# Optimization experiments

Measured on AMD Instinct MI355X. Metric: run time of the kernel, lower is better.

## Reference

```python
import jax, jax.numpy as jnp
import numpy as np
import math

DIM_K = 64  # head dim used for scaling
NEG = -1000000000.0

def setup_inputs() -> dict:
    key = jax.random.key(0)
    k1, k2, k3, k4 = jax.random.split(key, 4)
    B, H, S, D = 4, 16, 2048, 64
    return {
        "key": jax.random.normal(k1, (B, H, S, D), dtype=jnp.float32),
        "query": jax.random.normal(k2, (B, H, S, D), dtype=jnp.float32),
        "value": jax.random.normal(k3, (B, H, S, D), dtype=jnp.float32),
        "mask": jax.random.randint(k4, (B, S, S), 0, 2, dtype=jnp.int32),
    }

def reference(key, query, value, mask):
    # scores: [B,H,Sq,Sk]
    scores = jnp.einsum('bhqd,bhkd->bhqk', query, key) / math.sqrt(DIM_K)
    scores = jnp.where(mask[:, None, :, :] == 0, NEG, scores)
    attn = jax.nn.softmax(scores, axis=-1)  # dropout is identity in eval mode
    return jnp.einsum('bhqk,bhkd->bhqd', attn, value)
```

## Files before the change

### kernel.cpp

```cpp
#include <hip/hip_runtime.h>
#include <stdint.h>

#define B_ 4
#define H_ 16
#define S_ 2048
#define D_ 64
#define NKT (S_ / 64)

typedef __attribute__((ext_vector_type(8))) short bf16x8;
typedef __attribute__((ext_vector_type(4))) float f32x4;
typedef unsigned long long u64;
typedef unsigned int u32;

__device__ inline short f2bf(float f) {
  union { float f; u32 u; } x; x.f = f;
  u32 r = x.u + 0x7FFFu + ((x.u >> 16) & 1u);
  return (short)(r >> 16);
}
__device__ inline short4 f2bf4(float4 v) {
  short4 s; s.x = f2bf(v.x); s.y = f2bf(v.y); s.z = f2bf(v.z); s.w = f2bf(v.w);
  return s;
}
__device__ inline short f2bf_fast(float f) {
  union { float f; u32 u; } x; x.f = f;
  return (short)((x.u + 0x8000u) >> 16);
}

__device__ inline int SW(int row, int byteoff) {
  return row * 128 + (byteoff ^ ((row & 7) << 4));
}

__device__ inline void gll16(const void* g, void* l) {
  __builtin_amdgcn_global_load_lds(
      (const __attribute__((address_space(1))) u32*)g,
      (__attribute__((address_space(3))) u32*)(uintptr_t)l, 16, 0, 0);
}


__global__ void pack_mask(const int* __restrict__ M, u64* __restrict__ P) {
  int idx = blockIdx.x * 256 + threadIdx.x;
  int v = M[idx];
  u64 bits = __ballot(v != 0);
  if ((threadIdx.x & 63) == 0) P[idx >> 6] = bits;
}

__global__ void convK(const float* __restrict__ Kg, char* __restrict__ Ksw) {
  int idx = blockIdx.x * 256 + threadIdx.x;
  int row = idx >> 4, c4 = idx & 15;
  float4 v = *(const float4*)(Kg + (size_t)idx * 4);
  *(short4*)(Ksw + (size_t)row * 128 + ((c4 * 8) ^ ((row & 7) << 4))) = f2bf4(v);
}

__global__ void convV(const float* __restrict__ Vg, char* __restrict__ Vsw) {
  __shared__ short tile[4096];
  char* ct = (char*)tile;
  int tid = threadIdx.x;
  int bh = blockIdx.x >> 5, kt = blockIdx.x & 31;
  int c4 = tid & 15, g = tid >> 4;
  const float* src = Vg + (size_t)bh * (S_ * D_) + (size_t)(kt * 64 + g * 4) * D_ + c4 * 4;
  float4 vv[4];
#pragma unroll
  for (int i = 0; i < 4; ++i) vv[i] = *(const float4*)(src + (size_t)i * D_);
  const float* vf = (const float*)vv;
#pragma unroll
  for (int dd = 0; dd < 4; ++dd) {
    short4 s;
    s.x = f2bf(vf[0 * 4 + dd]);
    s.y = f2bf(vf[1 * 4 + dd]);
    s.z = f2bf(vf[2 * 4 + dd]);
    s.w = f2bf(vf[3 * 4 + dd]);
    *(short4*)(ct + SW(c4 * 4 + dd, g * 8)) = s;
  }
  __syncthreads();
  char* dst = Vsw + (size_t)blockIdx.x * 8192;
#pragma unroll
  for (int j = 0; j < 2; ++j)
    *(float4*)(dst + tid * 16 + j * 4096) = *(const float4*)(ct + tid * 16 + j * 4096);
}


__global__ __launch_bounds__(256, 4)
void attn_kernel(const float* __restrict__ Qg,
                 const char* __restrict__ Ksw,
                 const char* __restrict__ Vsw,
                 const u64* __restrict__ Mp,
                 float* __restrict__ Og) {
  __shared__ short sK[2][4096];
  __shared__ short sV[2][4096];
  __shared__ short sP[4096];

  const int tid  = threadIdx.x;
  const int w    = tid >> 6;
  const int lane = tid & 63;
  const int quad = lane >> 4;
  const int c    = lane & 15;
  const int bh   = blockIdx.y;
  const int b    = bh >> 4;
  const int q0   = blockIdx.x * 64;
  const size_t base = (size_t)bh * (S_ * D_);
  const char* Kt = Ksw + (size_t)bh * (S_ * 128);
  const char* Vt = Vsw + (size_t)bh * (S_ * 128);
  char* cP = (char*)sP;

  const float SC = 0.125f * 1.44269504088896f;
#pragma unroll
  for (int j = 0; j < 4; ++j) {
    int idx = tid + j * 256;
    int row = idx >> 4, c4 = idx & 15;
    float4 v = *(const float4*)(Qg + base + (size_t)(q0 + row) * D_ + c4 * 4);
    v.x *= SC; v.y *= SC; v.z *= SC; v.w *= SC;
    *(short4*)(cP + SW(row, c4 * 8)) = f2bf4(v);
  }
#pragma unroll
  for (int j = 0; j < 2; ++j) {
    gll16(Kt + tid * 16 + j * 4096, (char*)sK[0] + tid * 16 + j * 4096);
    gll16(Vt + tid * 16 + j * 4096, (char*)sV[0] + tid * 16 + j * 4096);
  }
  __syncthreads();
  bf16x8 qa0 = *(bf16x8*)(cP + SW(16 * w + c, quad * 16));
  bf16x8 qa1 = *(bf16x8*)(cP + SW(16 * w + c, 64 + quad * 16));

  f32x4 acco[4] = {f32x4{0,0,0,0}, f32x4{0,0,0,0}, f32x4{0,0,0,0}, f32x4{0,0,0,0}};
  float l_run[4] = {0.f, 0.f, 0.f, 0.f};

  const u64* mrow = Mp + ((size_t)b * S_ + q0 + 16 * w + quad * 4) * NKT;

  for (int kt = 0; kt < NKT; ++kt) {
    const char* cK = (const char*)sK[kt & 1];
    const char* cV = (const char*)sV[kt & 1];

    __syncthreads();

    if (kt + 1 < NKT) {
      char* kn = (char*)sK[(kt + 1) & 1];
      char* vn = (char*)sV[(kt + 1) & 1];
      const char* kg = Kt + (size_t)(kt + 1) * 8192;
      const char* vg = Vt + (size_t)(kt + 1) * 8192;
#pragma unroll
      for (int j = 0; j < 2; ++j) {
        gll16(kg + tid * 16 + j * 4096, kn + tid * 16 + j * 4096);
        gll16(vg + tid * 16 + j * 4096, vn + tid * 16 + j * 4096);
      }
    }

    u64 mw[4];
#pragma unroll
    for (int r = 0; r < 4; ++r) mw[r] = mrow[(size_t)r * NKT + kt];

    f32x4 accs[4];
#pragma unroll
    for (int n = 0; n < 4; ++n) {
      bf16x8 kb0 = *(bf16x8*)(cK + SW(16 * n + c, quad * 16));
      bf16x8 kb1 = *(bf16x8*)(cK + SW(16 * n + c, 64 + quad * 16));
      f32x4 z = {0, 0, 0, 0};
      z = __builtin_amdgcn_mfma_f32_16x16x32_bf16(qa0, kb0, z, 0, 0, 0);
      z = __builtin_amdgcn_mfma_f32_16x16x32_bf16(qa1, kb1, z, 0, 0, 0);
      accs[n] = z;
    }

#pragma unroll
    for (int r = 0; r < 4; ++r) {
      unsigned mlo = (unsigned)(mw[r]) >> c;
      unsigned mhi = (unsigned)(mw[r] >> 32) >> c;
      float e0 = (mlo & 1u)         ? exp2f(accs[0][r]) : 0.0f;
      float e1 = ((mlo >> 16) & 1u) ? exp2f(accs[1][r]) : 0.0f;
      float e2 = (mhi & 1u)         ? exp2f(accs[2][r]) : 0.0f;
      float e3 = ((mhi >> 16) & 1u) ? exp2f(accs[3][r]) : 0.0f;
      accs[0][r] = e0; accs[1][r] = e1; accs[2][r] = e2; accs[3][r] = e3;
      float rs = (e0 + e1) + (e2 + e3);
      rs += __shfl_xor(rs, 1);
      rs += __shfl_xor(rs, 2);
      rs += __shfl_xor(rs, 4);
      rs += __shfl_xor(rs, 8);
      l_run[r] += rs;
    }

#pragma unroll
    for (int r = 0; r < 4; ++r)
#pragma unroll
      for (int n = 0; n < 4; ++n)
        *(short*)(cP + SW(16 * w + quad * 4 + r, (16 * n + c) * 2)) = f2bf_fast(accs[n][r]);

    bf16x8 pa0 = *(bf16x8*)(cP + SW(16 * w + c, quad * 16));
    bf16x8 pa1 = *(bf16x8*)(cP + SW(16 * w + c, 64 + quad * 16));

#pragma unroll
    for (int dn = 0; dn < 4; ++dn) {
      bf16x8 vb0 = *(bf16x8*)(cV + SW(16 * dn + c, quad * 16));
      bf16x8 vb1 = *(bf16x8*)(cV + SW(16 * dn + c, 64 + quad * 16));
      acco[dn] = __builtin_amdgcn_mfma_f32_16x16x32_bf16(pa0, vb0, acco[dn], 0, 0, 0);
      acco[dn] = __builtin_amdgcn_mfma_f32_16x16x32_bf16(pa1, vb1, acco[dn], 0, 0, 0);
    }
  }

#pragma unroll
  for (int r = 0; r < 4; ++r) {
    float inv = 1.0f / l_run[r];
    size_t orow = base + (size_t)(q0 + 16 * w + quad * 4 + r) * D_;
#pragma unroll
    for (int dn = 0; dn < 4; ++dn)
      Og[orow + 16 * dn + c] = acco[dn][r] * inv;
  }
}

extern "C" void kernel_launch(void* const* d_in, const int* in_sizes, int n_in,
                              void* d_out, int out_size, void* d_ws, size_t ws_size,
                              hipStream_t stream) {
  const float* Kg = (const float*)d_in[0];
  const float* Qg = (const float*)d_in[1];
  const float* Vg = (const float*)d_in[2];
  const int*   Mg = (const int*)d_in[3];
  float* Og = (float*)d_out;

  char* ws  = (char*)d_ws;
  u64*  Mp  = (u64*)ws;
  char* Ksw = ws + (size_t)(2u << 20);
  char* Vsw = ws + (size_t)(2u << 20) + (16u << 20);

  pack_mask<<<(B_ * S_ * S_) / 256, 256, 0, stream>>>(Mg, Mp);
  convK<<<(B_ * H_ * S_ * 16) / 256, 256, 0, stream>>>(Kg, Ksw);
  convV<<<B_ * H_ * NKT, 256, 0, stream>>>(Vg, Vsw);
  attn_kernel<<<dim3(S_ / 64, B_ * H_), 256, 0, stream>>>(Qg, Ksw, Vsw, Mp, Og);
}
```

Baseline: 368.0 us.

## Double query tile per block and merge preprocessing kernels into one launch

Each attention block now handles 128 query rows, with every wave working on two 16-row groups. Each K/V tile loaded into shared memory therefore serves twice as many queries, halving K/V traffic per query and the number of barriers per query. Row-sum shuffles are moved out of the inner loop to the epilogue, and mask words are prefetched one tile ahead. The three prepass kernels are fused into a single launch to cut launch overhead, at the cost of more registers and shared memory per block, lower occupancy (launch bounds 3) and half as many blocks.

```diff
diff --git a/kernel.cpp b/kernel.cpp
--- a/kernel.cpp
+++ b/kernel.cpp
@@ -6,6 +6,7 @@
 #define S_ 2048
 #define D_ 64
 #define NKT (S_ / 64)
+#define QM 128
 
 typedef __attribute__((ext_vector_type(8))) short bf16x8;
 typedef __attribute__((ext_vector_type(4))) float f32x4;
@@ -36,50 +37,53 @@
       (__attribute__((address_space(3))) u32*)(uintptr_t)l, 16, 0, 0);
 }
 
-
-__global__ void pack_mask(const int* __restrict__ M, u64* __restrict__ P) {
-  int idx = blockIdx.x * 256 + threadIdx.x;
-  int v = M[idx];
-  u64 bits = __ballot(v != 0);
-  if ((threadIdx.x & 63) == 0) P[idx >> 6] = bits;
-}
-
-__global__ void convK(const float* __restrict__ Kg, char* __restrict__ Ksw) {
-  int idx = blockIdx.x * 256 + threadIdx.x;
-  int row = idx >> 4, c4 = idx & 15;
-  float4 v = *(const float4*)(Kg + (size_t)idx * 4);
-  *(short4*)(Ksw + (size_t)row * 128 + ((c4 * 8) ^ ((row & 7) << 4))) = f2bf4(v);
-}
-
-__global__ void convV(const float* __restrict__ Vg, char* __restrict__ Vsw) {
+__global__ __launch_bounds__(256)
+void prepass(const float* __restrict__ Kg, const float* __restrict__ Vg,
+             const int* __restrict__ Mg,
+             char* __restrict__ Ksw, char* __restrict__ Vsw, u64* __restrict__ Mp) {
   __shared__ short tile[4096];
-  char* ct = (char*)tile;
-  int tid = threadIdx.x;
-  int bh = blockIdx.x >> 5, kt = blockIdx.x & 31;
-  int c4 = tid & 15, g = tid >> 4;
-  const float* src = Vg + (size_t)bh * (S_ * D_) + (size_t)(kt * 64 + g * 4) * D_ + c4 * 4;
-  float4 vv[4];
-#pragma unroll
-  for (int i = 0; i < 4; ++i) vv[i] = *(const float4*)(src + (size_t)i * D_);
-  const float* vf = (const float*)vv;
-#pragma unroll
-  for (int dd = 0; dd < 4; ++dd) {
-    short4 s;
-    s.x = f2bf(vf[0 * 4 + dd]);
-    s.y = f2bf(vf[1 * 4 + dd]);
-    s.z = f2bf(vf[2 * 4 + dd]);
-    s.w = f2bf(vf[3 * 4 + dd]);
-    *(short4*)(ct + SW(c4 * 4 + dd, g * 8)) = s;
-  }
-  __syncthreads();
-  char* dst = Vsw + (size_t)blockIdx.x * 8192;
-#pragma unroll
-  for (int j = 0; j < 2; ++j)
-    *(float4*)(dst + tid * 16 + j * 4096) = *(const float4*)(ct + tid * 16 + j * 4096);
-}
-
-
-__global__ __launch_bounds__(256, 4)
+  const int bid = blockIdx.x, tid = threadIdx.x;
+  if (bid < 8192) {
+    int idx = bid * 256 + tid;
+    int row = idx >> 4, c4 = idx & 15;
+    float4 v = *(const float4*)(Kg + (size_t)idx * 4);
+    *(short4*)(Ksw + (size_t)row * 128 + ((c4 * 8) ^ ((row & 7) << 4))) = f2bf4(v);
+  } else if (bid < 10240) {
+    int vb = bid - 8192;
+    char* ct = (char*)tile;
+    int c4 = tid & 15, g = tid >> 4;
+    const float* src = Vg + (size_t)vb * (64 * D_) + (size_t)(g * 4) * D_ + c4 * 4;
+    float4 vv[4];
+#pragma unroll
+    for (int i = 0; i < 4; ++i) vv[i] = *(const float4*)(src + (size_t)i * D_);
+    const float* vf = (const float*)vv;
+#pragma unroll
+    for (int dd = 0; dd < 4; ++dd) {
+      short4 s;
+      s.x = f2bf(vf[0 * 4 + dd]);
+      s.y = f2bf(vf[1 * 4 + dd]);
+      s.z = f2bf(vf[2 * 4 + dd]);
+      s.w = f2bf(vf[3 * 4 + dd]);
+      *(short4*)(ct + SW(c4 * 4 + dd, g * 8)) = s;
+    }
+    __syncthreads();
+    char* dst = Vsw + (size_t)vb * 8192;
+#pragma unroll
+    for (int j = 0; j < 2; ++j)
+      *(float4*)(dst + tid * 16 + j * 4096) = *(const float4*)(ct + tid * 16 + j * 4096);
+  } else {
+    int pb = bid - 10240;
+    int gbase = pb * 1024;
+#pragma unroll
+    for (int j = 0; j < 4; ++j) {
+      int idx = gbase + j * 256 + tid;
+      u64 bits = __ballot(Mg[idx] != 0);
+      if ((tid & 63) == 0) Mp[idx >> 6] = bits;
+    }
+  }
+}
+
+__global__ __launch_bounds__(256, 3)
 void attn_kernel(const float* __restrict__ Qg,
                  const char* __restrict__ Ksw,
                  const char* __restrict__ Vsw,
@@ -87,7 +91,7 @@
                  float* __restrict__ Og) {
   __shared__ short sK[2][4096];
   __shared__ short sV[2][4096];
-  __shared__ short sP[4096];
+  __shared__ short sP[8192];
 
   const int tid  = threadIdx.x;
   const int w    = tid >> 6;
@@ -96,7 +100,7 @@
   const int c    = lane & 15;
   const int bh   = blockIdx.y;
   const int b    = bh >> 4;
-  const int q0   = blockIdx.x * 64;
+  const int q0   = blockIdx.x * QM;
   const size_t base = (size_t)bh * (S_ * D_);
   const char* Kt = Ksw + (size_t)bh * (S_ * 128);
   const char* Vt = Vsw + (size_t)bh * (S_ * 128);
@@ -104,7 +108,7 @@
 
   const float SC = 0.125f * 1.44269504088896f;
 #pragma unroll
-  for (int j = 0; j < 4; ++j) {
+  for (int j = 0; j < 8; ++j) {
     int idx = tid + j * 256;
     int row = idx >> 4, c4 = idx & 15;
     float4 v = *(const float4*)(Qg + base + (size_t)(q0 + row) * D_ + c4 * 4);
@@ -117,13 +121,30 @@
     gll16(Vt + tid * 16 + j * 4096, (char*)sV[0] + tid * 16 + j * 4096);
   }
   __syncthreads();
-  bf16x8 qa0 = *(bf16x8*)(cP + SW(16 * w + c, quad * 16));
-  bf16x8 qa1 = *(bf16x8*)(cP + SW(16 * w + c, 64 + quad * 16));
-
-  f32x4 acco[4] = {f32x4{0,0,0,0}, f32x4{0,0,0,0}, f32x4{0,0,0,0}, f32x4{0,0,0,0}};
-  float l_run[4] = {0.f, 0.f, 0.f, 0.f};
-
-  const u64* mrow = Mp + ((size_t)b * S_ + q0 + 16 * w + quad * 4) * NKT;
+
+  bf16x8 qa[2][2];
+#pragma unroll
+  for (int gi = 0; gi < 2; ++gi) {
+    qa[gi][0] = *(bf16x8*)(cP + SW(32 * w + 16 * gi + c, quad * 16));
+    qa[gi][1] = *(bf16x8*)(cP + SW(32 * w + 16 * gi + c, 64 + quad * 16));
+  }
+
+  f32x4 acco[2][4];
+  float l_part[2][4];
+#pragma unroll
+  for (int gi = 0; gi < 2; ++gi)
+#pragma unroll
+    for (int i = 0; i < 4; ++i) { acco[gi][i] = f32x4{0,0,0,0}; l_part[gi][i] = 0.f; }
+
+  const u64* mrow[2];
+  mrow[0] = Mp + ((size_t)b * S_ + q0 + 32 * w + quad * 4) * NKT;
+  mrow[1] = mrow[0] + 16 * NKT;
+
+  u64 mw[2][4];
+#pragma unroll
+  for (int gi = 0; gi < 2; ++gi)
+#pragma unroll
+    for (int r = 0; r < 4; ++r) mw[gi][r] = mrow[gi][(size_t)r * NKT];
 
   for (int kt = 0; kt < NKT; ++kt) {
     const char* cK = (const char*)sK[kt & 1];
@@ -142,64 +163,84 @@
         gll16(vg + tid * 16 + j * 4096, vn + tid * 16 + j * 4096);
       }
     }
-
-    u64 mw[4];
-#pragma unroll
-    for (int r = 0; r < 4; ++r) mw[r] = mrow[(size_t)r * NKT + kt];
-
-    f32x4 accs[4];
+    const int ktn = (kt + 1 < NKT) ? kt + 1 : kt;
+    u64 mwn[2][4];
+#pragma unroll
+    for (int gi = 0; gi < 2; ++gi)
+#pragma unroll
+      for (int r = 0; r < 4; ++r) mwn[gi][r] = mrow[gi][(size_t)r * NKT + ktn];
+
+    f32x4 accs[2][4];
 #pragma unroll
     for (int n = 0; n < 4; ++n) {
       bf16x8 kb0 = *(bf16x8*)(cK + SW(16 * n + c, quad * 16));
       bf16x8 kb1 = *(bf16x8*)(cK + SW(16 * n + c, 64 + quad * 16));
-      f32x4 z = {0, 0, 0, 0};
-      z = __builtin_amdgcn_mfma_f32_16x16x32_bf16(qa0, kb0, z, 0, 0, 0);
-      z = __builtin_amdgcn_mfma_f32_16x16x32_bf16(qa1, kb1, z, 0, 0, 0);
-      accs[n] = z;
-    }
-
-#pragma unroll
-    for (int r = 0; r < 4; ++r) {
-      unsigned mlo = (unsigned)(mw[r]) >> c;
-      unsigned mhi = (unsigned)(mw[r] >> 32) >> c;
-      float e0 = (mlo & 1u)         ? exp2f(accs[0][r]) : 0.0f;
-      float e1 = ((mlo >> 16) & 1u) ? exp2f(accs[1][r]) : 0.0f;
-      float e2 = (mhi & 1u)         ? exp2f(accs[2][r]) : 0.0f;
-      float e3 = ((mhi >> 16) & 1u) ? exp2f(accs[3][r]) : 0.0f;
-      accs[0][r] = e0; accs[1][r] = e1; accs[2][r] = e2; accs[3][r] = e3;
-      float rs = (e0 + e1) + (e2 + e3);
-      rs += __shfl_xor(rs, 1);
-      rs += __shfl_xor(rs, 2);
-      rs += __shfl_xor(rs, 4);
-      rs += __shfl_xor(rs, 8);
-      l_run[r] += rs;
-    }
-
-#pragma unroll
-    for (int r = 0; r < 4; ++r)
-#pragma unroll
-      for (int n = 0; n < 4; ++n)
-        *(short*)(cP + SW(16 * w + quad * 4 + r, (16 * n + c) * 2)) = f2bf_fast(accs[n][r]);
-
-    bf16x8 pa0 = *(bf16x8*)(cP + SW(16 * w + c, quad * 16));
-    bf16x8 pa1 = *(bf16x8*)(cP + SW(16 * w + c, 64 + quad * 16));
+#pragma unroll
+      for (int gi = 0; gi < 2; ++gi) {
+        f32x4 z = {0, 0, 0, 0};
+        z = __builtin_amdgcn_mfma_f32_16x16x32_bf16(qa[gi][0], kb0, z, 0, 0, 0);
+        z = __builtin_amdgcn_mfma_f32_16x16x32_bf16(qa[gi][1], kb1, z, 0, 0, 0);
+        accs[gi][n] = z;
+      }
+    }
+
+#pragma unroll
+    for (int gi = 0; gi < 2; ++gi) {
+#pragma unroll
+      for (int r = 0; r < 4; ++r) {
+        unsigned mlo = (unsigned)(mw[gi][r]) >> c;
+        unsigned mhi = (unsigned)(mw[gi][r] >> 32) >> c;
+        float e0 = (mlo & 1u)         ? exp2f(accs[gi][0][r]) : 0.0f;
+        float e1 = ((mlo >> 16) & 1u) ? exp2f(accs[gi][1][r]) : 0.0f;
+        float e2 = (mhi & 1u)         ? exp2f(accs[gi][2][r]) : 0.0f;
+        float e3 = ((mhi >> 16) & 1u) ? exp2f(accs[gi][3][r]) : 0.0f;
+        l_part[gi][r] += (e0 + e1) + (e2 + e3);
+        int prow = 32 * w + 16 * gi + quad * 4 + r;
+        *(short*)(cP + SW(prow, (c) * 2))      = f2bf_fast(e0);
+        *(short*)(cP + SW(prow, (16 + c) * 2)) = f2bf_fast(e1);
+        *(short*)(cP + SW(prow, (32 + c) * 2)) = f2bf_fast(e2);
+        *(short*)(cP + SW(prow, (48 + c) * 2)) = f2bf_fast(e3);
+      }
+    }
+#pragma unroll
+    for (int gi = 0; gi < 2; ++gi)
+#pragma unroll
+      for (int r = 0; r < 4; ++r) mw[gi][r] = mwn[gi][r];
+
+    bf16x8 pa[2][2];
+#pragma unroll
+    for (int gi = 0; gi < 2; ++gi) {
+      pa[gi][0] = *(bf16x8*)(cP + SW(32 * w + 16 * gi + c, quad * 16));
+      pa[gi][1] = *(bf16x8*)(cP + SW(32 * w + 16 * gi + c, 64 + quad * 16));
+    }
 
 #pragma unroll
     for (int dn = 0; dn < 4; ++dn) {
       bf16x8 vb0 = *(bf16x8*)(cV + SW(16 * dn + c, quad * 16));
       bf16x8 vb1 = *(bf16x8*)(cV + SW(16 * dn + c, 64 + quad * 16));
-      acco[dn] = __builtin_amdgcn_mfma_f32_16x16x32_bf16(pa0, vb0, acco[dn], 0, 0, 0);
-      acco[dn] = __builtin_amdgcn_mfma_f32_16x16x32_bf16(pa1, vb1, acco[dn], 0, 0, 0);
-    }
-  }
-
-#pragma unroll
-  for (int r = 0; r < 4; ++r) {
-    float inv = 1.0f / l_run[r];
-    size_t orow = base + (size_t)(q0 + 16 * w + quad * 4 + r) * D_;
-#pragma unroll
-    for (int dn = 0; dn < 4; ++dn)
-      Og[orow + 16 * dn + c] = acco[dn][r] * inv;
+#pragma unroll
+      for (int gi = 0; gi < 2; ++gi) {
+        acco[gi][dn] = __builtin_amdgcn_mfma_f32_16x16x32_bf16(pa[gi][0], vb0, acco[gi][dn], 0, 0, 0);
+        acco[gi][dn] = __builtin_amdgcn_mfma_f32_16x16x32_bf16(pa[gi][1], vb1, acco[gi][dn], 0, 0, 0);
+      }
+    }
+  }
+
+#pragma unroll
+  for (int gi = 0; gi < 2; ++gi) {
+#pragma unroll
+    for (int r = 0; r < 4; ++r) {
+      float l = l_part[gi][r];
+      l += __shfl_xor(l, 1);
+      l += __shfl_xor(l, 2);
+      l += __shfl_xor(l, 4);
+      l += __shfl_xor(l, 8);
+      float inv = 1.0f / l;
+      size_t orow = base + (size_t)(q0 + 32 * w + 16 * gi + quad * 4 + r) * D_;
+#pragma unroll
+      for (int dn = 0; dn < 4; ++dn)
+        Og[orow + 16 * dn + c] = acco[gi][dn][r] * inv;
+    }
   }
 }
 
@@ -217,8 +258,6 @@
   char* Ksw = ws + (size_t)(2u << 20);
   char* Vsw = ws + (size_t)(2u << 20) + (16u << 20);
 
-  pack_mask<<<(B_ * S_ * S_) / 256, 256, 0, stream>>>(Mg, Mp);
-  convK<<<(B_ * H_ * S_ * 16) / 256, 256, 0, stream>>>(Kg, Ksw);
-  convV<<<B_ * H_ * NKT, 256, 0, stream>>>(Vg, Vsw);
-  attn_kernel<<<dim3(S_ / 64, B_ * H_), 256, 0, stream>>>(Qg, Ksw, Vsw, Mp, Og);
-}
+  prepass<<<26624, 256, 0, stream>>>(Kg, Vg, Mg, Ksw, Vsw, Mp);
+  attn_kernel<<<dim3(S_ / QM, B_ * H_), 256, 0, stream>>>(Qg, Ksw, Vsw, Mp, Og);
+}
```

After: 332.8 us. 1.11x faster.
